# Optimization experiments

Hardware: AMD Instinct MI355X
Metric: run time of the kernel (lower is better)

Reference implementation:

```python
import jax, jax.numpy as jnp
import numpy as np

N = 128                      # reduced state dimension (Q_dim[0])
S = N * (N + 1) // 2         # number of triu pairwise products = 8256
BATCH = 16384                # snapshot columns
_rows, _cols = np.triu_indices(N)
ROWS = jnp.asarray(_rows)    # [S] int32 constants
COLS = jnp.asarray(_cols)


def setup_inputs() -> dict:
    key = jax.random.key(0)
    kx, ka, kb = jax.random.split(key, 3)
    x = jax.random.normal(kx, (N, BATCH), dtype=jnp.float32)
    # learned operators (module inits them to zeros; use small random for a meaningful baseline)
    A = jax.random.normal(ka, (N, N), dtype=jnp.float32) * 0.02
    B = jax.random.normal(kb, (N, S), dtype=jnp.float32) * 0.02
    return {"x": x, "A": A, "B": B}


def reference(x, A, B):
    # quadratic feature expansion: x2[k, :] = x[i_k, :] * x[j_k, :] over triu pairs
    x2 = x[ROWS] * x[COLS]                 # [S, BATCH]
    return A @ x + B @ x2                  # [N, BATCH]
```

## Files before the change

### kernel.cpp

```cpp
#include <hip/hip_runtime.h>


constexpr int N_     = 128;
constexpr int S_     = 8256;
constexpr int BATCH_ = 16384;
constexpr int KTOT   = 8384;
constexpr int NKT    = 131;
constexpr size_t WT_BYTES = (size_t)KTOT * 128 * 2;
constexpr size_t PP_OFF   = WT_BYTES;
constexpr size_t XH_OFF   = PP_OFF + 32768;

typedef __attribute__((ext_vector_type(8))) _Float16 half8;
typedef __attribute__((ext_vector_type(2))) _Float16 half2t;
typedef __attribute__((ext_vector_type(4))) float f32x4;

__device__ __forceinline__ ushort f2h(float f) {
    _Float16 h = (_Float16)f;
    ushort b; __builtin_memcpy(&b, &h, 2); return b;
}
__device__ __forceinline__ float h2f(ushort b) {
    _Float16 h; __builtin_memcpy(&h, &b, 2); return (float)h;
}
__device__ __forceinline__ half2t duph(ushort b) {
    uint w = ((uint)b << 16) | (uint)b;
    half2t d; __builtin_memcpy(&d, &w, 4); return d;
}
__device__ __forceinline__ half8 mul_bc(half8 w, half2t d) {
    union { half8 h; half2t p[4]; } u, r;
    u.h = w;
    #pragma unroll
    for (int q = 0; q < 4; ++q) r.p[q] = u.p[q] * d;
    return r.h;
}

__device__ __forceinline__ int cumN(int i) {
    if (i <= 0) return 0;
    const int n = i - 1, t = n >> 3, r = n & 7;
    return 16 * i - (4 * t * (t + 1) + r * (t + 1));
}
__device__ __forceinline__ int offR(int i) {
    const int a = i >> 3, b = i & 7;
    const int p = b ? (8 * (b - 1) - (((b - 1) * b) >> 1)) : 0;
    return 28 * a + p;
}
__device__ __forceinline__ int triS(int i) { return i * (257 - i) / 2; }

__global__ __launch_bounds__(256) void build_all(
    const float* __restrict__ x,
    const float* __restrict__ A, const float* __restrict__ B,
    ushort* __restrict__ pp, ushort* __restrict__ wt,
    ushort* __restrict__ xh, float* __restrict__ out)
{
    const int bid = blockIdx.x, t = threadIdx.x;
    if (bid < 524) {
        const int idx = bid * 256 + t;
        const int ko  = idx >> 7;
        const int m   = idx & 127;
        const int kt = ko >> 3, kk = (ko >> 2) & 1, oct = ko & 3;
        const int lane = oct * 16 + (m & 15);
        const int e0 = kt * 8192 + kk * 4096 + (m >> 6) * 2048 +
                       ((m >> 4) & 3) * 512 + lane * 8;
        float v[8];
        if (ko < 16) {
            const int i0 = ko * 8;
            #pragma unroll
            for (int el = 0; el < 8; ++el) v[el] = A[m * 128 + i0 + el];
        } else if (ko < 992) {
            const int o = ko - 16;
            int i = 0;
            #pragma unroll
            for (int st = 64; st >= 1; st >>= 1) {
                const int c = i + st;
                if (c < 128 && cumN(c) <= o) i = c;
            }
            const int jb = ((i + 7) >> 3) + (o - cumN(i));
            const int s0 = triS(i) + jb * 8 - i;
            const float* bp = B + (size_t)m * S_ + s0;
            #pragma unroll
            for (int el = 0; el < 8; ++el) v[el] = bp[el];
        } else {
            const int kb = ko * 8 - 7936;
            #pragma unroll
            for (int el = 0; el < 8; ++el) {
                const int kloc = kb + el;
                int i = 0;
                #pragma unroll
                for (int st = 64; st >= 1; st >>= 1) {
                    const int c = i + st;
                    if (c < 128 && offR(c) <= kloc) i = c;
                }
                v[el] = B[(size_t)m * S_ + triS(i) + (kloc - offR(i))];
            }
        }
        ushort o8[8];
        #pragma unroll
        for (int el = 0; el < 8; ++el) o8[el] = f2h(v[el]);
        __builtin_memcpy(wt + e0, o8, 16);
    } else if (bid < 780) {
        const int zb = bid - 524;
        f32x4* o4 = (f32x4*)out;
        #pragma unroll
        for (int c = 0; c < 4; ++c)
            o4[(size_t)zb * 2048 + c * 512 + t] = (f32x4){0.f, 0.f, 0.f, 0.f};
    } else if (bid == 780) {
        const int i = t;
        if (i < 128) {
            pp[i] = (ushort)(i | (0xFFu << 8));
            const int jb0 = (i + 7) >> 3;
            int kb = 128 + cumN(i) * 8;
            for (int jb = jb0; jb < 16; ++jb) {
                #pragma unroll
                for (int e = 0; e < 8; ++e)
                    pp[kb + e] = (ushort)(i | ((jb * 8 + e) << 8));
                kb += 8;
            }
            const int h = (8 - (i & 7)) & 7;
            const int rb = 7936 + offR(i);
            for (int e = 0; e < h; ++e)
                pp[rb + e] = (ushort)(i | ((i + e) << 8));
        }
    } else {
        const int col = (bid - 781) * 256 + t;
        ushort* xc = xh + (size_t)col * 128;
        const int cs = col & 15;
        #pragma unroll
        for (int ro = 0; ro < 16; ++ro) {
            uint ow[4];
            #pragma unroll
            for (int p = 0; p < 4; ++p) {
                const ushort u0 = f2h(x[(size_t)(ro * 8 + 2 * p) * BATCH_ + col]);
                const ushort u1 = f2h(x[(size_t)(ro * 8 + 2 * p + 1) * BATCH_ + col]);
                ow[p] = (uint)u0 | ((uint)u1 << 16);
            }
            __builtin_memcpy(xc + ((ro ^ cs) << 3), ow, 16);
        }
    }
}

__device__ __forceinline__ void load_af(half8 af[8], const ushort* __restrict__ wt,
                                        int kt, int wm, int lane) {
    const ushort* ab = wt + ((size_t)kt << 13) + (wm << 11) + (lane << 3);
    #pragma unroll
    for (int kk = 0; kk < 2; ++kk)
        #pragma unroll
        for (int mt = 0; mt < 4; ++mt)
            af[kk * 4 + mt] = *(const half8*)(ab + (kk << 12) + (mt << 9));
}

__device__ __forceinline__ void read_bin(ushort xi[2][4], half8 wj[2][4],
                                         uint w0, uint w1,
                                         const ushort* __restrict__ xbase,
                                         int sw) {
    const int ia = (int)(w0 & 0xFFu) ^ sw, ja = (int)((w0 >> 8) & 0xFFu) ^ sw;
    const int ib = (int)(w1 & 0xFFu) ^ sw, jb = (int)((w1 >> 8) & 0xFFu) ^ sw;
    #pragma unroll
    for (int nt = 0; nt < 4; ++nt) {
        const ushort* xb = xbase + nt * 2048;
        xi[0][nt] = xb[ia];
        xi[1][nt] = xb[ib];
        wj[0][nt] = *(const half8*)(xb + ja);
        wj[1][nt] = *(const half8*)(xb + jb);
    }
}

__device__ __forceinline__ void mfma_step(f32x4 acc[4][4], const half8 af[8],
                                          const ushort xi[2][4],
                                          const half8 wj[2][4]) {
    half8 bfr[2][4];
    #pragma unroll
    for (int kk = 0; kk < 2; ++kk)
        #pragma unroll
        for (int nt = 0; nt < 4; ++nt)
            bfr[kk][nt] = mul_bc(wj[kk][nt], duph(xi[kk][nt]));
    __builtin_amdgcn_s_setprio(1);
    #pragma unroll
    for (int kk = 0; kk < 2; ++kk)
        #pragma unroll
        for (int nt = 0; nt < 4; ++nt)
            #pragma unroll
            for (int mt = 0; mt < 4; ++mt)
                acc[mt][nt] = __builtin_amdgcn_mfma_f32_16x16x32_f16(
                    af[kk * 4 + mt], bfr[kk][nt], acc[mt][nt], 0, 0, 0);
    __builtin_amdgcn_s_setprio(0);
}

__global__ __launch_bounds__(512) void gemm_mfma(
    const ushort* __restrict__ xh,
    const ushort* __restrict__ wt,
    const ushort* __restrict__ pp,
    float* __restrict__ out)
{
    __shared__ ushort xt[256 * 128];

    const int t    = threadIdx.x;
    const int b0   = blockIdx.x * 256;
    const int sp   = blockIdx.y;
    const int kt0  = sp * 33;
    const int kt1  = (sp == 3) ? NKT : kt0 + 33;
    const int lane = t & 63;
    const int w    = t >> 6;
    const int wm   = w >> 2, wn = w & 3;
    const int l16  = lane & 15, quad = lane >> 4;
    const int sw   = l16 << 3;

    {
        const ushort* src = xh + (size_t)b0 * 128;
        #pragma unroll
        for (int i = 0; i < 8; ++i)
            *(half8*)(xt + i * 4096 + t * 8) =
                *(const half8*)(src + i * 4096 + t * 8);
    }
    __syncthreads();

    f32x4 acc[4][4];
    #pragma unroll
    for (int mt = 0; mt < 4; ++mt)
        #pragma unroll
        for (int nt = 0; nt < 4; ++nt)
            acc[mt][nt] = (f32x4){0.f, 0.f, 0.f, 0.f};

    const ushort* xbase = xt + (wn * 64 + l16) * 128;

    if (sp == 0) {
        for (int kt = 0; kt < 2; ++kt) {
            half8 af[8];
            load_af(af, wt, kt, wm, lane);
            #pragma unroll
            for (int kk = 0; kk < 2; ++kk) {
                const int off = (kt * 64 + kk * 32 + quad * 8) ^ sw;
                #pragma unroll
                for (int nt = 0; nt < 4; ++nt) {
                    const half8 bfr = *(const half8*)(xbase + nt * 2048 + off);
                    #pragma unroll
                    for (int mt = 0; mt < 4; ++mt)
                        acc[mt][nt] = __builtin_amdgcn_mfma_f32_16x16x32_f16(
                            af[kk * 4 + mt], bfr, acc[mt][nt], 0, 0, 0);
                }
            }
        }
    }

    {
        const int s_ni = (kt0 > 2) ? kt0 : 2;
        const int e_ni = (kt1 < 124) ? kt1 : 124;
        const int len  = e_ni - s_ni;
        if (len > 0) {
            int kt  = s_ni + ((w * len) >> 3);
            int ktn = (kt + 1 < e_ni) ? kt + 1 : s_ni;

            half8  afA[8], afB[8];
            ushort xiA[2][4], xiB[2][4];
            half8  wjA[2][4], wjB[2][4];

            const uint c0 = *(const uint*)(pp + kt * 64 + quad * 8);
            const uint c1 = *(const uint*)(pp + kt * 64 + 32 + quad * 8);
            load_af(afA, wt, kt, wm, lane);
            uint n0 = *(const uint*)(pp + ktn * 64 + quad * 8);
            uint n1 = *(const uint*)(pp + ktn * 64 + 32 + quad * 8);
            read_bin(xiA, wjA, c0, c1, xbase, sw);

            int rem = len;
            while (true) {
                {
                    const int kt2 = (ktn + 1 < e_ni) ? ktn + 1 : s_ni;
                    const uint m0 = *(const uint*)(pp + kt2 * 64 + quad * 8);
                    const uint m1 = *(const uint*)(pp + kt2 * 64 + 32 + quad * 8);
                    load_af(afB, wt, ktn, wm, lane);
                    read_bin(xiB, wjB, n0, n1, xbase, sw);
                    mfma_step(acc, afA, xiA, wjA);
                    n0 = m0; n1 = m1; ktn = kt2;
                    if (--rem == 0) break;
                }
                {
                    const int kt2 = (ktn + 1 < e_ni) ? ktn + 1 : s_ni;
                    const uint m0 = *(const uint*)(pp + kt2 * 64 + quad * 8);
                    const uint m1 = *(const uint*)(pp + kt2 * 64 + 32 + quad * 8);
                    load_af(afA, wt, ktn, wm, lane);
                    read_bin(xiA, wjA, n0, n1, xbase, sw);
                    mfma_step(acc, afB, xiB, wjB);
                    n0 = m0; n1 = m1; ktn = kt2;
                    if (--rem == 0) break;
                }
            }
        }
    }

    if (sp == 3) {
        for (int kt = 124; kt < NKT; ++kt) {
            half8 af[8];
            load_af(af, wt, kt, wm, lane);
            #pragma unroll
            for (int kk = 0; kk < 2; ++kk) {
                const int k0 = kt * 64 + kk * 32 + quad * 8;
                const uint4 pk = *(const uint4*)(pp + k0);
                const uint pr4[4] = {pk.x, pk.y, pk.z, pk.w};
                #pragma unroll
                for (int nt = 0; nt < 4; ++nt) {
                    const ushort* xb = xbase + nt * 2048;
                    float prods[8];
                    #pragma unroll
                    for (int e = 0; e < 8; ++e) {
                        const uint ent = (pr4[e >> 1] >> ((e & 1) * 16)) & 0xFFFFu;
                        prods[e] = h2f(xb[(int)(ent & 0xFFu) ^ sw]) *
                                   h2f(xb[(int)(ent >> 8) ^ sw]);
                    }
                    union { half8 h; uint wdw[4]; } bb;
                    #pragma unroll
                    for (int p = 0; p < 4; ++p) {
                        const auto pk2 = __builtin_amdgcn_cvt_pkrtz(
                            prods[2 * p], prods[2 * p + 1]);
                        __builtin_memcpy(&bb.wdw[p], &pk2, 4);
                    }
                    const half8 bfr = bb.h;
                    #pragma unroll
                    for (int mt = 0; mt < 4; ++mt)
                        acc[mt][nt] = __builtin_amdgcn_mfma_f32_16x16x32_f16(
                            af[kk * 4 + mt], bfr, acc[mt][nt], 0, 0, 0);
                }
            }
        }
    }

    #pragma unroll
    for (int mt = 0; mt < 4; ++mt) {
        #pragma unroll
        for (int nt = 0; nt < 4; ++nt) {
            const int mbase = wm * 64 + mt * 16 + quad * 4;
            const size_t col = (size_t)b0 + wn * 64 + nt * 16 + l16;
            #pragma unroll
            for (int r = 0; r < 4; ++r)
                unsafeAtomicAdd(&out[(size_t)(mbase + r) * BATCH_ + col],
                                acc[mt][nt][r]);
        }
    }
}

extern "C" void kernel_launch(void* const* d_in, const int* in_sizes, int n_in,
                              void* d_out, int out_size, void* d_ws, size_t ws_size,
                              hipStream_t stream) {
    const float* x = (const float*)d_in[0];
    const float* A = (const float*)d_in[1];
    const float* B = (const float*)d_in[2];
    float* out = (float*)d_out;

    ushort* wt = (ushort*)d_ws;
    ushort* pp = (ushort*)((char*)d_ws + PP_OFF);
    ushort* xh = (ushort*)((char*)d_ws + XH_OFF);

    build_all<<<845, 256, 0, stream>>>(x, A, B, pp, wt, xh, out);
    gemm_mfma<<<dim3(BATCH_ / 256, 4), 512, 0, stream>>>(xh, wt, pp, out);
}
```

Before: 121.5 us.

## Stage weight tiles into LDS with async global_load_lds double buffering

```diff
diff --git a/kernel.cpp b/kernel.cpp
--- a/kernel.cpp
+++ b/kernel.cpp
@@ -13,6 +13,9 @@
 typedef __attribute__((ext_vector_type(8))) _Float16 half8;
 typedef __attribute__((ext_vector_type(2))) _Float16 half2t;
 typedef __attribute__((ext_vector_type(4))) float f32x4;
+
+typedef __attribute__((address_space(1))) const unsigned int gas_u32;
+typedef __attribute__((address_space(3))) unsigned int las_u32;
 
 __device__ __forceinline__ ushort f2h(float f) {
     _Float16 h = (_Float16)f;
@@ -137,6 +140,16 @@
     }
 }
 
+__device__ __forceinline__ void gload_lds16(const ushort* g, ushort* l) {
+    __builtin_amdgcn_global_load_lds((gas_u32*)g, (las_u32*)l, 16, 0, 0);
+}
+__device__ __forceinline__ void stage_af(ushort* buf, const ushort* __restrict__ wt,
+                                         int kt, int t) {
+    const ushort* g = wt + ((size_t)kt << 13) + t * 8;
+    gload_lds16(g, buf + t * 8);
+    gload_lds16(g + 4096, buf + t * 8 + 4096);
+}
+
 __device__ __forceinline__ void load_af(half8 af[8], const ushort* __restrict__ wt,
                                         int kt, int wm, int lane) {
     const ushort* ab = wt + ((size_t)kt << 13) + (wm << 11) + (lane << 3);
@@ -191,6 +204,7 @@
     float* __restrict__ out)
 {
     __shared__ ushort xt[256 * 128];
+    __shared__ ushort afb[2][8192];
 
     const int t    = threadIdx.x;
     const int b0   = blockIdx.x * 256;
@@ -203,6 +217,9 @@
     const int l16  = lane & 15, quad = lane >> 4;
     const int sw   = l16 << 3;
 
+    const int s_ni = (kt0 > 2) ? kt0 : 2;
+    const int e_ni = (kt1 < 124) ? kt1 : 124;
+
     {
         const ushort* src = xh + (size_t)b0 * 128;
         #pragma unroll
@@ -210,7 +227,7 @@
             *(half8*)(xt + i * 4096 + t * 8) =
                 *(const half8*)(src + i * 4096 + t * 8);
     }
-    __syncthreads();
+    stage_af(&afb[0][0], wt, s_ni, t);
 
     f32x4 acc[4][4];
     #pragma unroll
@@ -218,6 +235,8 @@
         #pragma unroll
         for (int nt = 0; nt < 4; ++nt)
             acc[mt][nt] = (f32x4){0.f, 0.f, 0.f, 0.f};
+
+    __syncthreads();
 
     const ushort* xbase = xt + (wn * 64 + l16) * 128;
 
@@ -241,47 +260,31 @@
     }
 
     {
-        const int s_ni = (kt0 > 2) ? kt0 : 2;
-        const int e_ni = (kt1 < 124) ? kt1 : 124;
-        const int len  = e_ni - s_ni;
-        if (len > 0) {
-            int kt  = s_ni + ((w * len) >> 3);
-            int ktn = (kt + 1 < e_ni) ? kt + 1 : s_ni;
-
-            half8  afA[8], afB[8];
-            ushort xiA[2][4], xiB[2][4];
-            half8  wjA[2][4], wjB[2][4];
-
-            const uint c0 = *(const uint*)(pp + kt * 64 + quad * 8);
-            const uint c1 = *(const uint*)(pp + kt * 64 + 32 + quad * 8);
-            load_af(afA, wt, kt, wm, lane);
-            uint n0 = *(const uint*)(pp + ktn * 64 + quad * 8);
-            uint n1 = *(const uint*)(pp + ktn * 64 + 32 + quad * 8);
-            read_bin(xiA, wjA, c0, c1, xbase, sw);
-
-            int rem = len;
-            while (true) {
-                {
-                    const int kt2 = (ktn + 1 < e_ni) ? ktn + 1 : s_ni;
-                    const uint m0 = *(const uint*)(pp + kt2 * 64 + quad * 8);
-                    const uint m1 = *(const uint*)(pp + kt2 * 64 + 32 + quad * 8);
-                    load_af(afB, wt, ktn, wm, lane);
-                    read_bin(xiB, wjB, n0, n1, xbase, sw);
-                    mfma_step(acc, afA, xiA, wjA);
-                    n0 = m0; n1 = m1; ktn = kt2;
-                    if (--rem == 0) break;
-                }
-                {
-                    const int kt2 = (ktn + 1 < e_ni) ? ktn + 1 : s_ni;
-                    const uint m0 = *(const uint*)(pp + kt2 * 64 + quad * 8);
-                    const uint m1 = *(const uint*)(pp + kt2 * 64 + 32 + quad * 8);
-                    load_af(afA, wt, ktn, wm, lane);
-                    read_bin(xiA, wjA, n0, n1, xbase, sw);
-                    mfma_step(acc, afB, xiB, wjB);
-                    n0 = m0; n1 = m1; ktn = kt2;
-                    if (--rem == 0) break;
-                }
-            }
+        int cur = 0;
+        uint w0 = *(const uint*)(pp + s_ni * 64 + quad * 8);
+        uint w1 = *(const uint*)(pp + s_ni * 64 + 32 + quad * 8);
+        for (int kt = s_ni; kt < e_ni; ++kt) {
+            const int ktn = (kt + 1 < e_ni) ? kt + 1 : kt;
+            if (kt + 1 < e_ni) stage_af(&afb[cur ^ 1][0], wt, kt + 1, t);
+            const uint nw0 = *(const uint*)(pp + ktn * 64 + quad * 8);
+            const uint nw1 = *(const uint*)(pp + ktn * 64 + 32 + quad * 8);
+
+            const ushort* ab = &afb[cur][0] + (wm << 11) + (lane << 3);
+            half8 af[8];
+            #pragma unroll
+            for (int kk = 0; kk < 2; ++kk)
+                #pragma unroll
+                for (int mt = 0; mt < 4; ++mt)
+                    af[kk * 4 + mt] = *(const half8*)(ab + (kk << 12) + (mt << 9));
+
+            ushort xi[2][4]; half8 wj[2][4];
+            read_bin(xi, wj, w0, w1, xbase, sw);
+
+            mfma_step(acc, af, xi, wj);
+
+            w0 = nw0; w1 = nw1;
+            __syncthreads();
+            cur ^= 1;
         }
     }
 
```

Measured after the change: 137.6 us. +13.2%, slower.
